# Optimization experiments

Measured on AMD Instinct MI355X. Metric: run time of the kernel, lower is better.

The kernel has to match this reference:

```python
import jax, jax.numpy as jnp
import numpy as np

B, N_NODES, T_IN = 512, 32, 12
HID, HEADS, OUT_CH, DEG = 64, 8, 9, 8


def setup_inputs() -> dict:
    key = jax.random.key(0)
    ks = jax.random.split(key, 26)
    rn = lambda k, s, sc=0.1: (jax.random.normal(k, s, jnp.float32) * sc)
    E = B * N_NODES * DEG
    src = jax.random.randint(ks[0], (E,), 0, N_NODES, jnp.int32)
    dst = jax.random.randint(ks[1], (E,), 0, N_NODES, jnp.int32)
    off = jnp.repeat(jnp.arange(B, dtype=jnp.int32) * N_NODES, N_NODES * DEG)
    edge_index = jnp.stack([src + off, dst + off])  # block-diagonal batched graph
    x = jax.random.normal(ks[2], (B, N_NODES, T_IN), jnp.float32)
    return {
        "x": x,
        "edge_index": edge_index,
        # gat1: in=T_IN -> HEADS*HID, concat
        "W1": rn(ks[3], (T_IN, HEADS * HID)),
        "a_src1": rn(ks[4], (HEADS, HID)),
        "a_dst1": rn(ks[5], (HEADS, HID)),
        "b1": rn(ks[6], (HEADS * HID,), 0.01),
        # gat2: in=HEADS*HID -> HID, heads=1, mean (concat=False)
        "W2": rn(ks[7], (HEADS * HID, HID), 0.05),
        "a_src2": rn(ks[8], (1, HID)),
        "a_dst2": rn(ks[9], (1, HID)),
        "b2": rn(ks[10], (HID,), 0.01),
        "gamma": jnp.ones((HID,), jnp.float32),
        "beta": jnp.zeros((HID,), jnp.float32),
        # gru1: input_size=N_NODES(=32), hidden=HID
        "Wi1": rn(ks[11], (3 * HID, N_NODES)),
        "Wh1": rn(ks[12], (3 * HID, HID)),
        "bi1": rn(ks[13], (3 * HID,), 0.01),
        "bh1": rn(ks[14], (3 * HID,), 0.01),
        # gru2: input_size=HID, hidden=HID
        "Wi2": rn(ks[15], (3 * HID, HID)),
        "Wh2": rn(ks[16], (3 * HID, HID)),
        "bi2": rn(ks[17], (3 * HID,), 0.01),
        "bh2": rn(ks[18], (3 * HID,), 0.01),
        "Wf": rn(ks[19], (OUT_CH, HID)),
        "bf": rn(ks[20], (OUT_CH,), 0.01),
    }


def _gat_layer(x, src, dst, W, a_s, a_d, b, concat):
    # PyG GATConv (eval mode, self-loops already appended by caller)
    Nn = x.shape[0]
    heads, hc = a_s.shape
    h = (x @ W).reshape(Nn, heads, hc)                 # [N, H, C]
    es = jnp.sum(h * a_s, axis=-1)                     # [N, H]
    ed = jnp.sum(h * a_d, axis=-1)
    e = jax.nn.leaky_relu(es[src] + ed[dst], 0.2)      # [E, H]
    m = jax.ops.segment_max(e, dst, num_segments=Nn)
    p = jnp.exp(e - m[dst])
    s = jax.ops.segment_sum(p, dst, num_segments=Nn)
    alpha = p / (s[dst] + 1e-16)                       # per-dst softmax
    out = jax.ops.segment_sum(h[src] * alpha[:, :, None], dst, num_segments=Nn)
    out = out.reshape(Nn, heads * hc) if concat else out.mean(axis=1)
    return out + b


def _gru(x, Wi, Wh, bi, bh):
    # torch.nn.GRU (batch_first) single layer; x: [B, T, F]
    H = Wh.shape[1]
    xi = x @ Wi.T + bi                                 # [B, T, 3H]
    def step(h, xt):
        gh = h @ Wh.T + bh
        r = jax.nn.sigmoid(xt[:, :H] + gh[:, :H])
        z = jax.nn.sigmoid(xt[:, H:2 * H] + gh[:, H:2 * H])
        n = jnp.tanh(xt[:, 2 * H:] + r * gh[:, 2 * H:])
        hn = (1.0 - z) * n + z * h
        return hn, hn
    h0 = jnp.zeros((x.shape[0], H), x.dtype)
    _, ys = jax.lax.scan(step, h0, jnp.swapaxes(xi, 0, 1))
    return jnp.swapaxes(ys, 0, 1)


def reference(x, edge_index, W1, a_src1, a_dst1, b1, W2, a_src2, a_dst2, b2,
              gamma, beta, Wi1, Wh1, bi1, bh1, Wi2, Wh2, bi2, bh2, Wf, bf):
    Bsz, Nn_, T = x.shape
    Nn = Bsz * Nn_
    xf = x.reshape(Nn, T)                              # dropout is identity in eval
    sl = jnp.arange(Nn, dtype=edge_index.dtype)        # PyG add_self_loops=True
    src = jnp.concatenate([edge_index[0], sl])
    dst = jnp.concatenate([edge_index[1], sl])
    h = jax.nn.elu(_gat_layer(xf, src, dst, W1, a_src1, a_dst1, b1, True))
    h = jax.nn.elu(_gat_layer(h, src, dst, W2, a_src2, a_dst2, b2, False))
    mu = h.mean(-1, keepdims=True)
    var = ((h - mu) ** 2).mean(-1, keepdims=True)
    h = (h - mu) / jnp.sqrt(var + 1e-5) * gamma + beta
    seq = h.reshape(Bsz, Nn_, -1).transpose(0, 2, 1)   # [B, HID(seq), N_NODES(feat)]
    g = _gru(seq, Wi1, Wh1, bi1, bh1)
    g = _gru(g, Wi2, Wh2, bi2, bh2)
    return g[:, -1, :] @ Wf.T + bf                     # [B, OUT_CH]
```

## Files before the change

### kernel.cpp

```cpp
#include <hip/hip_runtime.h>
#include <hip/hip_bf16.h>
#include <stdint.h>

#define BATCH 512
#define NN 32
#define T_IN 12
#define HID 64
#define HEADS 8
#define OUT_CH 9
#define EPB (NN*8)
#define ETOT (EPB+NN)
#define F1 (HEADS*HID)

using u16 = unsigned short;
using u32 = unsigned int;
typedef _Float16 f16;
typedef _Float16 f16x2 __attribute__((ext_vector_type(2)));
typedef u32 v4u __attribute__((ext_vector_type(4)));
typedef float v4f __attribute__((ext_vector_type(4)));

__device__ __forceinline__ float bf2f(u16 u){ return __uint_as_float(((u32)u)<<16); }
__device__ __forceinline__ u16 f2bf(float f){
    u32 x = __float_as_uint(f);
    u32 r = (x + 0x7FFFu + ((x>>16)&1u))>>16;
    return (u16)r;
}
__device__ __forceinline__ u32 packf16(float a, float b){
    f16x2 p; p.x=(f16)a; p.y=(f16)b; return __builtin_bit_cast(u32,p);
}
__device__ __forceinline__ u16 f2h16(float a){ f16 h=(f16)a; return __builtin_bit_cast(u16,h); }
__device__ __forceinline__ float h16f(u16 v){ f16 h=__builtin_bit_cast(f16,v); return (float)h; }
__device__ __forceinline__ float lof(u32 w){ return (float)__builtin_bit_cast(f16x2,w).x; }
__device__ __forceinline__ float hif(u32 w){ return (float)__builtin_bit_cast(f16x2,w).y; }
__device__ __forceinline__ float dot2(u32 a, u32 b, float c){
#if __has_builtin(__builtin_amdgcn_fdot2)
    return __builtin_amdgcn_fdot2(__builtin_bit_cast(f16x2,a), __builtin_bit_cast(f16x2,b), c, false);
#else
    return fmaf(lof(a),lof(b), fmaf(hif(a),hif(b), c));
#endif
}
__device__ __forceinline__ float elu1(float x){ return x > 0.f ? x : (__expf(x)-1.f); }
__device__ __forceinline__ float sigm(float x){ return 1.f/(1.f+__expf(-x)); }
__device__ __forceinline__ float tanh_(float x){ return 1.f - 2.f/(__expf(2.f*x)+1.f); }
__device__ __forceinline__ u32 fenc(float v){
    u32 b=__float_as_uint(v);
    return (b&0x80000000u) ? ~b : (b|0x80000000u);
}
__device__ __forceinline__ float fdec(u32 k){
    return __uint_as_float((k&0x80000000u) ? (k&0x7FFFFFFFu) : ~k);
}

#define DOT4(acc,A,W) do{ acc=dot2(A.x,W.x,acc); acc=dot2(A.y,W.y,acc); \
                          acc=dot2(A.z,W.z,acc); acc=dot2(A.w,W.w,acc); }while(0)

struct CvtDesc {
    const void* src[16];
    void*       dst[16];
    int         n[16];
};

__global__ __launch_bounds__(256) void k_setup(
    const u32* __restrict__ xw, CvtDesc d,
    const void* __restrict__ W2src, u16* __restrict__ W2i,
    const void* __restrict__ Wi1, const void* __restrict__ Wh1,
    const void* __restrict__ Wi2, const void* __restrict__ Wh2,
    u32* __restrict__ wpk, int* __restrict__ flag)
{
    __shared__ int cnt;
    if(threadIdx.x==0) cnt=0;
    __syncthreads();
    int c=0;
    for(int i=threadIdx.x;i<4096;i+=256){
        u32 w=xw[i];
        if(w & 0x7FFFFFFFu){
            u32 el=(w>>7)&0xFFu;
            if(el>=0x90u) c++;
        }
    }
    atomicAdd(&cnt,c);
    __syncthreads();
    const int f = (cnt>256) ? 1 : 0;
    if(blockIdx.x==0 && threadIdx.x==0) *flag=f;

    const int bk=blockIdx.x;
    if(bk<128){
        int seg=bk>>3, sub=bk&7;
        const void* s=d.src[seg];
        float* o=(float*)d.dst[seg];
        int n=d.n[seg];
        for(int i=sub*256+threadIdx.x;i<n;i+=2048)
            o[i] = f ? ((const float*)s)[i] : bf2f(((const u16*)s)[i]);
    } else if(bk<256){
        int i=(bk-128)*256+threadIdx.x;
        int k=i>>6, j=i&63;
        float v = f? ((const float*)W2src)[i] : bf2f(((const u16*)W2src)[i]);
        W2i[ (((size_t)(k>>3)*64 + j)<<3) + (k&7) ] = f2h16(v);
    } else {
        int w=(bk-256)*256+threadIdx.x;
        int m=w/6144;
        int rem=w-m*6144;
        int row=rem>>5, kw=rem&31;
        const void* s=(m==0)?Wi1:(m==1)?Wh1:(m==2)?Wi2:Wh2;
        int K=(m==0)?32:64;
        int k0=2*kw, k1=k0+1;
        float v0=0.f, v1=0.f;
        if(k0<K) v0 = f? ((const float*)s)[row*K+k0] : bf2f(((const u16*)s)[row*K+k0]);
        if(k1<K) v1 = f? ((const float*)s)[row*K+k1] : bf2f(((const u16*)s)[row*K+k1]);
        wpk[w]=packf16(v0,v1);
    }
}

__global__ __launch_bounds__(256,2) void k_gat1(
    const float* __restrict__ x, const int* __restrict__ ei,
    const float* __restrict__ W1, const float* __restrict__ a_s, const float* __restrict__ a_d,
    const float* __restrict__ b1, u32* __restrict__ h1g)
{
    const int b = blockIdx.x, t = threadIdx.x;
    __shared__ __align__(16) float s_x[NN][12];
    __shared__ float s_W1[T_IN*F1];
    __shared__ __align__(16) u16 s_h[NN][520];
    __shared__ __align__(16) u32 s_aspk[HEADS*32], s_adpk[HEADS*32];
    __shared__ float s_es[NN][HEADS], s_ed[NN][HEADS];
    __shared__ unsigned char s_src[ETOT], s_dst[ETOT];
    __shared__ float s_al[HEADS][ETOT];
    __shared__ u32 s_mx[NN*HEADS];
    __shared__ float s_sm[NN*HEADS], s_inv[NN*HEADS];
    __shared__ int s_cnt[NN], s_off[NN], s_fil[NN];
    __shared__ short s_lst[ETOT];

    for(int i=t;i<NN*T_IN;i+=256) s_x[i/12][i%12] = x[b*NN*T_IN + i];
    for(int i=t;i<T_IN*F1;i+=256) s_W1[i]=W1[i];
    s_aspk[t]=packf16(a_s[2*t],a_s[2*t+1]);
    s_adpk[t]=packf16(a_d[2*t],a_d[2*t+1]);
    s_mx[t]=0u; s_sm[t]=0.f;
    if(t<EPB){
        s_src[t] = (unsigned char)(ei[b*EPB+t] - b*NN);
        s_dst[t] = (unsigned char)(ei[(size_t)BATCH*EPB + b*EPB+t] - b*NN);
    }
    if(t<NN){ s_src[EPB+t]=s_dst[EPB+t]=(unsigned char)t; s_cnt[t]=0; s_fil[t]=0; }
    __syncthreads();

    {
        v4f Wa0,Wa1,Wa2,Wb0,Wb1,Wb2;
        Wa0.x=s_W1[0*F1+t]; Wa0.y=s_W1[1*F1+t]; Wa0.z=s_W1[2*F1+t]; Wa0.w=s_W1[3*F1+t];
        Wa1.x=s_W1[4*F1+t]; Wa1.y=s_W1[5*F1+t]; Wa1.z=s_W1[6*F1+t]; Wa1.w=s_W1[7*F1+t];
        Wa2.x=s_W1[8*F1+t]; Wa2.y=s_W1[9*F1+t]; Wa2.z=s_W1[10*F1+t]; Wa2.w=s_W1[11*F1+t];
        Wb0.x=s_W1[0*F1+t+256]; Wb0.y=s_W1[1*F1+t+256]; Wb0.z=s_W1[2*F1+t+256]; Wb0.w=s_W1[3*F1+t+256];
        Wb1.x=s_W1[4*F1+t+256]; Wb1.y=s_W1[5*F1+t+256]; Wb1.z=s_W1[6*F1+t+256]; Wb1.w=s_W1[7*F1+t+256];
        Wb2.x=s_W1[8*F1+t+256]; Wb2.y=s_W1[9*F1+t+256]; Wb2.z=s_W1[10*F1+t+256]; Wb2.w=s_W1[11*F1+t+256];
        for(int n=0;n<NN;n++){
            const float4* xp=(const float4*)s_x[n];
            float4 xa=xp[0], xb=xp[1], xc=xp[2];
            float A=0.f,B=0.f;
            A=fmaf(xa.x,Wa0.x,A); A=fmaf(xa.y,Wa0.y,A); A=fmaf(xa.z,Wa0.z,A); A=fmaf(xa.w,Wa0.w,A);
            A=fmaf(xb.x,Wa1.x,A); A=fmaf(xb.y,Wa1.y,A); A=fmaf(xb.z,Wa1.z,A); A=fmaf(xb.w,Wa1.w,A);
            A=fmaf(xc.x,Wa2.x,A); A=fmaf(xc.y,Wa2.y,A); A=fmaf(xc.z,Wa2.z,A); A=fmaf(xc.w,Wa2.w,A);
            B=fmaf(xa.x,Wb0.x,B); B=fmaf(xa.y,Wb0.y,B); B=fmaf(xa.z,Wb0.z,B); B=fmaf(xa.w,Wb0.w,B);
            B=fmaf(xb.x,Wb1.x,B); B=fmaf(xb.y,Wb1.y,B); B=fmaf(xb.z,Wb1.z,B); B=fmaf(xb.w,Wb1.w,B);
            B=fmaf(xc.x,Wb2.x,B); B=fmaf(xc.y,Wb2.y,B); B=fmaf(xc.z,Wb2.z,B); B=fmaf(xc.w,Wb2.w,B);
            s_h[n][t]=f2h16(A); s_h[n][t+256]=f2h16(B);
        }
    }
    for(int e=t;e<ETOT;e+=256) atomicAdd(&s_cnt[s_dst[e]],1);
    __syncthreads();

    {
        int n=t&31, hd=t>>5;
        const v4u* hp=(const v4u*)((const u16*)s_h[n] + hd*64);
        v4u h0=hp[0],h1=hp[1],h2=hp[2],h3=hp[3],h4=hp[4],h5=hp[5],h6=hp[6],h7=hp[7];
        const v4u* ap=(const v4u*)&s_aspk[hd*32];
        const v4u* dp=(const v4u*)&s_adpk[hd*32];
        float e1=0.f,e2=0.f;
        { v4u w=ap[0]; DOT4(e1,h0,w); w=ap[1]; DOT4(e1,h1,w); w=ap[2]; DOT4(e1,h2,w); w=ap[3]; DOT4(e1,h3,w);
          w=ap[4]; DOT4(e1,h4,w); w=ap[5]; DOT4(e1,h5,w); w=ap[6]; DOT4(e1,h6,w); w=ap[7]; DOT4(e1,h7,w); }
        { v4u w=dp[0]; DOT4(e2,h0,w); w=dp[1]; DOT4(e2,h1,w); w=dp[2]; DOT4(e2,h2,w); w=dp[3]; DOT4(e2,h3,w);
          w=dp[4]; DOT4(e2,h4,w); w=dp[5]; DOT4(e2,h5,w); w=dp[6]; DOT4(e2,h6,w); w=dp[7]; DOT4(e2,h7,w); }
        s_es[n][hd]=e1; s_ed[n][hd]=e2;
    }
    if(t==0){ int o=0; for(int i=0;i<NN;i++){ s_off[i]=o; o+=s_cnt[i]; } }
    __syncthreads();

    for(int e=t;e<ETOT;e+=256){
        int d=s_dst[e]; int p=atomicAdd(&s_fil[d],1); s_lst[s_off[d]+p]=(short)e;
    }
    for(int i=t;i<ETOT*HEADS;i+=256){
        int hd=i/ETOT, e=i-hd*ETOT;
        int sr=s_src[e], d=s_dst[e];
        float v = s_es[sr][hd]+s_ed[d][hd];
        v = v>0.f? v : 0.2f*v;
        s_al[hd][e]=v;
        atomicMax(&s_mx[d*8+hd], fenc(v));
    }
    __syncthreads();

    for(int i=t;i<ETOT*HEADS;i+=256){
        int hd=i/ETOT, e=i-hd*ETOT;
        int d=s_dst[e];
        float p=__expf(s_al[hd][e]-fdec(s_mx[d*8+hd]));
        s_al[hd][e]=p;
        atomicAdd(&s_sm[d*8+hd], p);
    }
    __syncthreads();
    s_inv[t]=1.f/(s_sm[t]+1e-16f);
    __syncthreads();

    {
        int d=t&31, hd=t>>5;
        int o=s_off[d], cnt=s_cnt[d];
        float inv=s_inv[d*8+hd];
        size_t obase = ((size_t)(b*NN+d))*256 + hd*32;
        #pragma unroll
        for(int ch=0;ch<2;ch++){
            v4f a0=0,a1=0,a2=0,a3=0,a4=0,a5=0,a6=0,a7=0;
            for(int i=0;i<cnt;i++){
                int e=s_lst[o+i]; float av=s_al[hd][e]; int sr=s_src[e];
                const v4u* hp=(const v4u*)((const u16*)s_h[sr] + hd*64 + ch*32);
                v4u p0=hp[0],p1=hp[1],p2=hp[2],p3=hp[3];
                a0.x=fmaf(av,lof(p0.x),a0.x); a0.y=fmaf(av,hif(p0.x),a0.y);
                a0.z=fmaf(av,lof(p0.y),a0.z); a0.w=fmaf(av,hif(p0.y),a0.w);
                a1.x=fmaf(av,lof(p0.z),a1.x); a1.y=fmaf(av,hif(p0.z),a1.y);
                a1.z=fmaf(av,lof(p0.w),a1.z); a1.w=fmaf(av,hif(p0.w),a1.w);
                a2.x=fmaf(av,lof(p1.x),a2.x); a2.y=fmaf(av,hif(p1.x),a2.y);
                a2.z=fmaf(av,lof(p1.y),a2.z); a2.w=fmaf(av,hif(p1.y),a2.w);
                a3.x=fmaf(av,lof(p1.z),a3.x); a3.y=fmaf(av,hif(p1.z),a3.y);
                a3.z=fmaf(av,lof(p1.w),a3.z); a3.w=fmaf(av,hif(p1.w),a3.w);
                a4.x=fmaf(av,lof(p2.x),a4.x); a4.y=fmaf(av,hif(p2.x),a4.y);
                a4.z=fmaf(av,lof(p2.y),a4.z); a4.w=fmaf(av,hif(p2.y),a4.w);
                a5.x=fmaf(av,lof(p2.z),a5.x); a5.y=fmaf(av,hif(p2.z),a5.y);
                a5.z=fmaf(av,lof(p2.w),a5.z); a5.w=fmaf(av,hif(p2.w),a5.w);
                a6.x=fmaf(av,lof(p3.x),a6.x); a6.y=fmaf(av,hif(p3.x),a6.y);
                a6.z=fmaf(av,lof(p3.y),a6.z); a6.w=fmaf(av,hif(p3.y),a6.w);
                a7.x=fmaf(av,lof(p3.z),a7.x); a7.y=fmaf(av,hif(p3.z),a7.y);
                a7.z=fmaf(av,lof(p3.w),a7.z); a7.w=fmaf(av,hif(p3.w),a7.w);
            }
            const float* bp = b1 + hd*64 + ch*32;
            u32* op = h1g + obase + ch*16;
            op[0] = packf16(elu1(a0.x*inv+bp[0]),  elu1(a0.y*inv+bp[1]));
            op[1] = packf16(elu1(a0.z*inv+bp[2]),  elu1(a0.w*inv+bp[3]));
            op[2] = packf16(elu1(a1.x*inv+bp[4]),  elu1(a1.y*inv+bp[5]));
            op[3] = packf16(elu1(a1.z*inv+bp[6]),  elu1(a1.w*inv+bp[7]));
            op[4] = packf16(elu1(a2.x*inv+bp[8]),  elu1(a2.y*inv+bp[9]));
            op[5] = packf16(elu1(a2.z*inv+bp[10]), elu1(a2.w*inv+bp[11]));
            op[6] = packf16(elu1(a3.x*inv+bp[12]), elu1(a3.y*inv+bp[13]));
            op[7] = packf16(elu1(a3.z*inv+bp[14]), elu1(a3.w*inv+bp[15]));
            op[8] = packf16(elu1(a4.x*inv+bp[16]), elu1(a4.y*inv+bp[17]));
            op[9] = packf16(elu1(a4.z*inv+bp[18]), elu1(a4.w*inv+bp[19]));
            op[10]= packf16(elu1(a5.x*inv+bp[20]), elu1(a5.y*inv+bp[21]));
            op[11]= packf16(elu1(a5.z*inv+bp[22]), elu1(a5.w*inv+bp[23]));
            op[12]= packf16(elu1(a6.x*inv+bp[24]), elu1(a6.y*inv+bp[25]));
            op[13]= packf16(elu1(a6.z*inv+bp[26]), elu1(a6.w*inv+bp[27]));
            op[14]= packf16(elu1(a7.x*inv+bp[28]), elu1(a7.y*inv+bp[29]));
            op[15]= packf16(elu1(a7.z*inv+bp[30]), elu1(a7.w*inv+bp[31]));
        }
    }
}

__global__ __launch_bounds__(256,2) void k_gat2ln(
    const u32* __restrict__ h1g, const int* __restrict__ ei,
    const uint4* __restrict__ W2i, const float* __restrict__ a_s2, const float* __restrict__ a_d2,
    const float* __restrict__ b2, const float* __restrict__ gam, const float* __restrict__ bet,
    float* __restrict__ hlng)
{
    const int b=blockIdx.x, t=threadIdx.x;
    __shared__ __align__(16) u32 s_h1[NN*260];
    __shared__ float s_h2[NN][HID];
    __shared__ float s_es[NN], s_ed[NN];
    __shared__ unsigned char s_src[ETOT], s_dst[ETOT];
    __shared__ float s_al[ETOT];
    __shared__ u32 s_mx[NN];
    __shared__ float s_sm[NN], s_inv[NN];
    __shared__ int s_cnt[NN], s_off[NN], s_fil[NN];
    __shared__ short s_lst[ETOT];

    { const u32* g = h1g + (size_t)b*8192;
      for(int w=t; w<8192; w+=256){ int n=w>>8, c=w&255; s_h1[n*260+c]=g[w]; } }
    if(t<EPB){
        s_src[t]=(unsigned char)(ei[b*EPB+t]-b*NN);
        s_dst[t]=(unsigned char)(ei[(size_t)BATCH*EPB+b*EPB+t]-b*NN);
    }
    if(t<NN){ s_src[EPB+t]=s_dst[EPB+t]=(unsigned char)t;
              s_cnt[t]=0; s_fil[t]=0; s_mx[t]=0u; s_sm[t]=0.f; }
    __syncthreads();

    for(int e=t;e<ETOT;e+=256) atomicAdd(&s_cnt[s_dst[e]],1);
    {
        int n0=(t>>5)<<2, j0=(t&31)<<1;
        const u32* r0=&s_h1[(n0+0)*260];
        const u32* r1=&s_h1[(n0+1)*260];
        const u32* r2=&s_h1[(n0+2)*260];
        const u32* r3=&s_h1[(n0+3)*260];
        float a00=0,a01=0,a10=0,a11=0,a20=0,a21=0,a30=0,a31=0;
        for(int kb=0;kb<64;kb++){
            uint4 A0=*(const uint4*)&r0[kb*4];
            uint4 A1=*(const uint4*)&r1[kb*4];
            uint4 A2=*(const uint4*)&r2[kb*4];
            uint4 A3=*(const uint4*)&r3[kb*4];
            const uint4* wp=&W2i[kb*64+j0];
            uint4 w0=wp[0], w1=wp[1];
            a00=dot2(A0.x,w0.x,a00); a00=dot2(A0.y,w0.y,a00); a00=dot2(A0.z,w0.z,a00); a00=dot2(A0.w,w0.w,a00);
            a01=dot2(A0.x,w1.x,a01); a01=dot2(A0.y,w1.y,a01); a01=dot2(A0.z,w1.z,a01); a01=dot2(A0.w,w1.w,a01);
            a10=dot2(A1.x,w0.x,a10); a10=dot2(A1.y,w0.y,a10); a10=dot2(A1.z,w0.z,a10); a10=dot2(A1.w,w0.w,a10);
            a11=dot2(A1.x,w1.x,a11); a11=dot2(A1.y,w1.y,a11); a11=dot2(A1.z,w1.z,a11); a11=dot2(A1.w,w1.w,a11);
            a20=dot2(A2.x,w0.x,a20); a20=dot2(A2.y,w0.y,a20); a20=dot2(A2.z,w0.z,a20); a20=dot2(A2.w,w0.w,a20);
            a21=dot2(A2.x,w1.x,a21); a21=dot2(A2.y,w1.y,a21); a21=dot2(A2.z,w1.z,a21); a21=dot2(A2.w,w1.w,a21);
            a30=dot2(A3.x,w0.x,a30); a30=dot2(A3.y,w0.y,a30); a30=dot2(A3.z,w0.z,a30); a30=dot2(A3.w,w0.w,a30);
            a31=dot2(A3.x,w1.x,a31); a31=dot2(A3.y,w1.y,a31); a31=dot2(A3.z,w1.z,a31); a31=dot2(A3.w,w1.w,a31);
        }
        s_h2[n0+0][j0]=a00; s_h2[n0+0][j0+1]=a01;
        s_h2[n0+1][j0]=a10; s_h2[n0+1][j0+1]=a11;
        s_h2[n0+2][j0]=a20; s_h2[n0+2][j0+1]=a21;
        s_h2[n0+3][j0]=a30; s_h2[n0+3][j0+1]=a31;
    }
    __syncthreads();

    {
        int n=t>>3, g=t&7;
        float e1=0,e2=0;
        #pragma unroll
        for(int cc=0; cc<8; cc++){
            float hv = s_h2[n][g*8+cc];
            e1 += hv*a_s2[g*8+cc];
            e2 += hv*a_d2[g*8+cc];
        }
        #pragma unroll
        for(int m=1;m<8;m<<=1){ e1 += __shfl_xor(e1,m,64); e2 += __shfl_xor(e2,m,64); }
        if(g==0){ s_es[n]=e1; s_ed[n]=e2; }
    }
    if(t==0){ int o=0; for(int i=0;i<NN;i++){ s_off[i]=o; o+=s_cnt[i]; } }
    __syncthreads();

    for(int e=t;e<ETOT;e+=256){
        int d=s_dst[e]; int p=atomicAdd(&s_fil[d],1); s_lst[s_off[d]+p]=(short)e;
    }
    for(int e=t;e<ETOT;e+=256){
        int d=s_dst[e];
        float v = s_es[s_src[e]] + s_ed[d];
        v = v>0.f? v:0.2f*v;
        s_al[e]=v;
        atomicMax(&s_mx[d], fenc(v));
    }
    __syncthreads();

    for(int e=t;e<ETOT;e+=256){
        int d=s_dst[e];
        float p=__expf(s_al[e]-fdec(s_mx[d]));
        s_al[e]=p;
        atomicAdd(&s_sm[d], p);
    }
    __syncthreads();
    if(t<NN) s_inv[t]=1.f/(s_sm[t]+1e-16f);
    __syncthreads();

    {
        int n=t>>3, g=t&7;
        v4f a0=0, a1=0;
        int o=s_off[n], cnt=s_cnt[n];
        float inv=s_inv[n];
        for(int i=0;i<cnt;i++){
            int e=s_lst[o+i]; float a=s_al[e]; int sr=s_src[e];
            const float4* hp=(const float4*)&s_h2[sr][g*8];
            float4 v0=hp[0], v1=hp[1];
            a0.x=fmaf(a,v0.x,a0.x); a0.y=fmaf(a,v0.y,a0.y); a0.z=fmaf(a,v0.z,a0.z); a0.w=fmaf(a,v0.w,a0.w);
            a1.x=fmaf(a,v1.x,a1.x); a1.y=fmaf(a,v1.y,a1.y); a1.z=fmaf(a,v1.z,a1.z); a1.w=fmaf(a,v1.w,a1.w);
        }
        const float* bp=b2+g*8;
        float v0=elu1(a0.x*inv+bp[0]), v1=elu1(a0.y*inv+bp[1]);
        float v2=elu1(a0.z*inv+bp[2]), v3=elu1(a0.w*inv+bp[3]);
        float v4=elu1(a1.x*inv+bp[4]), v5=elu1(a1.y*inv+bp[5]);
        float v6=elu1(a1.z*inv+bp[6]), v7=elu1(a1.w*inv+bp[7]);
        float sum=v0+v1+v2+v3+v4+v5+v6+v7;
        float sq=v0*v0+v1*v1+v2*v2+v3*v3+v4*v4+v5*v5+v6*v6+v7*v7;
        #pragma unroll
        for(int m=1;m<8;m<<=1){ sum+=__shfl_xor(sum,m,64); sq+=__shfl_xor(sq,m,64); }
        float mu = sum*(1.f/64.f);
        float var = sq*(1.f/64.f) - mu*mu;
        float rs = rsqrtf(var + 1e-5f);
        float* outp = hlng + (size_t)b*HID*NN;
        int c=g*8;
        outp[(c+0)*NN+n]=(v0-mu)*rs*gam[c+0]+bet[c+0];
        outp[(c+1)*NN+n]=(v1-mu)*rs*gam[c+1]+bet[c+1];
        outp[(c+2)*NN+n]=(v2-mu)*rs*gam[c+2]+bet[c+2];
        outp[(c+3)*NN+n]=(v3-mu)*rs*gam[c+3]+bet[c+3];
        outp[(c+4)*NN+n]=(v4-mu)*rs*gam[c+4]+bet[c+4];
        outp[(c+5)*NN+n]=(v5-mu)*rs*gam[c+5]+bet[c+5];
        outp[(c+6)*NN+n]=(v6-mu)*rs*gam[c+6]+bet[c+6];
        outp[(c+7)*NN+n]=(v7-mu)*rs*gam[c+7]+bet[c+7];
    }
}

__global__ __launch_bounds__(256,2) void k_gruf(
    const float* __restrict__ hlng, const u32* __restrict__ wpk,
    const float* __restrict__ bi1, const float* __restrict__ bh1,
    const float* __restrict__ bi2, const float* __restrict__ bh2,
    const float* __restrict__ Wf, const float* __restrict__ bfv,
    void* __restrict__ outp, const int* __restrict__ flag)
{
    const int b=blockIdx.x, t=threadIdx.x;
    const int wave=t>>6, lane=t&63;
    const int layer=wave>>1;
    const int ublk=wave&1;
    const int uu=lane&31, s=lane>>5;
    const int u=ublk*32+uu;

    __shared__ __align__(16) u32 s_x1[64*16];
    __shared__ __align__(16) u32 s_h1[2][32];
    __shared__ __align__(16) u32 s_h2[2][32];
    __shared__ float s_h2f[64];

    { const float2* g=(const float2*)(hlng + (size_t)b*2048);
      for(int w=t;w<1024;w+=256){ float2 v=g[w]; s_x1[w]=packf16(v.x,v.y); } }
    if(t<32){ s_h1[0][t]=0u; s_h1[1][t]=0u; s_h2[0][t]=0u; s_h2[1][t]=0u; }

    u32 wiR[16],wiZ[16],wiN[16],whR[16],whZ[16],whN[16];
    const u32* wiu = wpk + (size_t)(layer*2+0)*6144;
    const u32* whu = wpk + (size_t)(layer*2+1)*6144;
    if(layer==0){
        #pragma unroll
        for(int k=0;k<8;k++){
            wiR[k]=wiu[u*32+s*8+k];
            wiZ[k]=wiu[(64+u)*32+s*8+k];
            wiN[k]=wiu[(128+u)*32+s*8+k];
        }
        #pragma unroll
        for(int k=0;k<16;k++){
            whR[k]=whu[u*32+s*16+k];
            whZ[k]=whu[(64+u)*32+s*16+k];
            whN[k]=whu[(128+u)*32+s*16+k];
        }
    } else {
        #pragma unroll
        for(int k=0;k<16;k++){
            wiR[k]=wiu[u*32+s*16+k];
            wiZ[k]=wiu[(64+u)*32+s*16+k];
            wiN[k]=wiu[(128+u)*32+s*16+k];
            whR[k]=whu[u*32+s*16+k];
            whZ[k]=whu[(64+u)*32+s*16+k];
            whN[k]=whu[(128+u)*32+s*16+k];
        }
    }
    const float* bi = layer? bi2:bi1;
    const float* bh = layer? bh2:bh1;
    float br=bi[u]+bh[u], bz=bi[64+u]+bh[64+u], bxn=bi[128+u], bhn=bh[128+u];
    float h=0.f;
    __syncthreads();

    for(int it=0; it<=64; ++it){
        const int pb=(it-1)&1, cb=it&1;
        bool act;
        float pr=0.f,pz=0.f,pxn=0.f,phn=0.f;
        if(layer==0){
            act=(it<64);
            if(act){
                const u32* xp=&s_x1[it*16+s*8];
                const u32* hp=&s_h1[pb][s*16];
                #pragma unroll
                for(int k=0;k<8;k++){ u32 xv=xp[k]; pr=dot2(xv,wiR[k],pr); pz=dot2(xv,wiZ[k],pz); pxn=dot2(xv,wiN[k],pxn); }
                #pragma unroll
                for(int k=0;k<16;k++){ u32 hv=hp[k]; pr=dot2(hv,whR[k],pr); pz=dot2(hv,whZ[k],pz); phn=dot2(hv,whN[k],phn); }
            }
        } else {
            act=(it>=1);
            if(act){
                const u32* xp=&s_h1[pb][s*16];
                const u32* hp=&s_h2[pb][s*16];
                #pragma unroll
                for(int k=0;k<16;k++){
                    u32 xv=xp[k], hv=hp[k];
                    pr=dot2(xv,wiR[k],pr); pz=dot2(xv,wiZ[k],pz); pxn=dot2(xv,wiN[k],pxn);
                    pr=dot2(hv,whR[k],pr); pz=dot2(hv,whZ[k],pz); phn=dot2(hv,whN[k],phn);
                }
            }
        }
        if(act){
            pr  += __shfl_xor(pr ,32,64);
            pz  += __shfl_xor(pz ,32,64);
            pxn += __shfl_xor(pxn,32,64);
            phn += __shfl_xor(phn,32,64);
            float r=sigm(pr+br), z=sigm(pz+bz);
            float n=tanh_(pxn+bxn + r*(phn+bhn));
            h=(1.f-z)*n + z*h;
            if(s==0){
                u16 hv=f2h16(h);
                if(layer==0) ((u16*)s_h1[cb])[u]=hv;
                else { ((u16*)s_h2[cb])[u]=hv; if(it==64) s_h2f[u]=h; }
            }
        }
        __syncthreads();
    }

    if(t<OUT_CH){
        float acc=bfv[t];
        const float4* wp=(const float4*)(Wf + t*64);
        const float4* hp=(const float4*)s_h2f;
        #pragma unroll
        for(int k=0;k<16;k++){
            float4 w=wp[k], v=hp[k];
            acc += w.x*v.x + w.y*v.y + w.z*v.z + w.w*v.w;
        }
        if(*flag) ((float*)outp)[b*OUT_CH+t]=acc;
        else      ((u16*)outp)[b*OUT_CH+t]=f2bf(acc);
    }
}

extern "C" void kernel_launch(void* const* d_in, const int* in_sizes, int n_in,
                              void* d_out, int out_size, void* d_ws, size_t ws_size,
                              hipStream_t stream)
{
    char* ws=(char*)d_ws;
    int* flag = (int*)ws;
    float* cf = (float*)(ws + 256);
    float* c_x   = cf; cf+=196608;
    float* c_W1  = cf; cf+=6144;
    float* c_as1 = cf; cf+=512;
    float* c_ad1 = cf; cf+=512;
    float* c_b1  = cf; cf+=512;
    float* c_as2 = cf; cf+=64;
    float* c_ad2 = cf; cf+=64;
    float* c_b2  = cf; cf+=64;
    float* c_gam = cf; cf+=64;
    float* c_bet = cf; cf+=64;
    float* c_bi1 = cf; cf+=192;
    float* c_bh1 = cf; cf+=192;
    float* c_bi2 = cf; cf+=192;
    float* c_bh2 = cf; cf+=192;
    float* c_Wf  = cf; cf+=576;
    float* c_bf  = cf; cf+=9;
    uintptr_t p = ((uintptr_t)cf + 255) & ~(uintptr_t)255;
    u16* c_W2i = (u16*)p;
    p = (p + 32768*2 + 255) & ~(uintptr_t)255;
    u32* wpk = (u32*)p;
    p = (p + 24576*4 + 255) & ~(uintptr_t)255;
    u32* h1g = (u32*)p;
    p = (p + (size_t)BATCH*NN*256*4 + 255) & ~(uintptr_t)255;
    float* hlng = (float*)p;

    const int* ei = (const int*)d_in[1];

    CvtDesc d;
    const int srcIdx[16] = {0,2,3,4,5,7,8,9,10,11,14,15,18,19,20,21};
    void* dsts[16] = {c_x,c_W1,c_as1,c_ad1,c_b1,c_as2,c_ad2,c_b2,c_gam,c_bet,
                      c_bi1,c_bh1,c_bi2,c_bh2,c_Wf,c_bf};
    const int ns[16] = {196608,6144,512,512,512,64,64,64,64,64,
                        192,192,192,192,576,9};
    for(int i=0;i<16;i++){ d.src[i]=d_in[srcIdx[i]]; d.dst[i]=dsts[i]; d.n[i]=ns[i]; }

    k_setup  <<<dim3(352),dim3(256),0,stream>>>((const u32*)d_in[0], d,
                                                d_in[6], c_W2i,
                                                d_in[12], d_in[13], d_in[16], d_in[17],
                                                wpk, flag);
    k_gat1   <<<dim3(BATCH),dim3(256),0,stream>>>(c_x,ei,c_W1,c_as1,c_ad1,c_b1,h1g);
    k_gat2ln <<<dim3(BATCH),dim3(256),0,stream>>>(h1g,ei,(const uint4*)c_W2i,c_as2,c_ad2,c_b2,c_gam,c_bet,hlng);
    k_gruf   <<<dim3(BATCH),dim3(256),0,stream>>>(hlng, wpk, c_bi1,c_bh1,c_bi2,c_bh2,
                                                  c_Wf, c_bf, d_out, flag);
}
```

Before: 238.8 us.

## Fuse GAT1, GAT2+LayerNorm and GRU kernels into one per-graph kernel

Merges the three per-batch kernels into a single kernel that keeps intermediates (GAT1 output, normalized GAT2 output) in shared memory instead of round-tripping through global workspace. It reuses the edge CSR lists built for layer 1 in layer 2 and loads W1 straight from global into registers rather than staging it in shared memory. This removes two kernel launches and roughly the global write/read of the intermediate activations. The cost is a longer, heavier kernel with more register pressure (32-word result array) and more shared memory, which could lower occupancy.

```diff
diff --git a/kernel.cpp b/kernel.cpp
--- a/kernel.cpp
+++ b/kernel.cpp
@@ -29,7 +29,6 @@
     f16x2 p; p.x=(f16)a; p.y=(f16)b; return __builtin_bit_cast(u32,p);
 }
 __device__ __forceinline__ u16 f2h16(float a){ f16 h=(f16)a; return __builtin_bit_cast(u16,h); }
-__device__ __forceinline__ float h16f(u16 v){ f16 h=__builtin_bit_cast(f16,v); return (float)h; }
 __device__ __forceinline__ float lof(u32 w){ return (float)__builtin_bit_cast(f16x2,w).x; }
 __device__ __forceinline__ float hif(u32 w){ return (float)__builtin_bit_cast(f16x2,w).y; }
 __device__ __forceinline__ float dot2(u32 a, u32 b, float c){
@@ -110,14 +109,21 @@
     }
 }
 
-__global__ __launch_bounds__(256,2) void k_gat1(
+__global__ __launch_bounds__(256,2) void k_fused(
     const float* __restrict__ x, const int* __restrict__ ei,
     const float* __restrict__ W1, const float* __restrict__ a_s, const float* __restrict__ a_d,
-    const float* __restrict__ b1, u32* __restrict__ h1g)
+    const float* __restrict__ b1,
+    const uint4* __restrict__ W2i, const float* __restrict__ a_s2, const float* __restrict__ a_d2,
+    const float* __restrict__ b2, const float* __restrict__ gam, const float* __restrict__ bet,
+    const u32* __restrict__ wpk,
+    const float* __restrict__ bi1, const float* __restrict__ bh1,
+    const float* __restrict__ bi2, const float* __restrict__ bh2,
+    const float* __restrict__ Wf, const float* __restrict__ bfv,
+    void* __restrict__ outp, const int* __restrict__ flag)
 {
     const int b = blockIdx.x, t = threadIdx.x;
+
     __shared__ __align__(16) float s_x[NN][12];
-    __shared__ float s_W1[T_IN*F1];
     __shared__ __align__(16) u16 s_h[NN][520];
     __shared__ __align__(16) u32 s_aspk[HEADS*32], s_adpk[HEADS*32];
     __shared__ float s_es[NN][HEADS], s_ed[NN][HEADS];
@@ -127,9 +133,13 @@
     __shared__ float s_sm[NN*HEADS], s_inv[NN*HEADS];
     __shared__ int s_cnt[NN], s_off[NN], s_fil[NN];
     __shared__ short s_lst[ETOT];
+    __shared__ float s_h2[NN][HID];
+    __shared__ __align__(16) u32 s_x1[64*16];
+    __shared__ __align__(16) u32 s_g1[2][32];
+    __shared__ __align__(16) u32 s_g2[2][32];
+    __shared__ float s_h2f[64];
 
     for(int i=t;i<NN*T_IN;i+=256) s_x[i/12][i%12] = x[b*NN*T_IN + i];
-    for(int i=t;i<T_IN*F1;i+=256) s_W1[i]=W1[i];
     s_aspk[t]=packf16(a_s[2*t],a_s[2*t+1]);
     s_adpk[t]=packf16(a_d[2*t],a_d[2*t+1]);
     s_mx[t]=0u; s_sm[t]=0.f;
@@ -138,28 +148,26 @@
         s_dst[t] = (unsigned char)(ei[(size_t)BATCH*EPB + b*EPB+t] - b*NN);
     }
     if(t<NN){ s_src[EPB+t]=s_dst[EPB+t]=(unsigned char)t; s_cnt[t]=0; s_fil[t]=0; }
-    __syncthreads();
-
-    {
-        v4f Wa0,Wa1,Wa2,Wb0,Wb1,Wb2;
-        Wa0.x=s_W1[0*F1+t]; Wa0.y=s_W1[1*F1+t]; Wa0.z=s_W1[2*F1+t]; Wa0.w=s_W1[3*F1+t];
-        Wa1.x=s_W1[4*F1+t]; Wa1.y=s_W1[5*F1+t]; Wa1.z=s_W1[6*F1+t]; Wa1.w=s_W1[7*F1+t];
-        Wa2.x=s_W1[8*F1+t]; Wa2.y=s_W1[9*F1+t]; Wa2.z=s_W1[10*F1+t]; Wa2.w=s_W1[11*F1+t];
-        Wb0.x=s_W1[0*F1+t+256]; Wb0.y=s_W1[1*F1+t+256]; Wb0.z=s_W1[2*F1+t+256]; Wb0.w=s_W1[3*F1+t+256];
-        Wb1.x=s_W1[4*F1+t+256]; Wb1.y=s_W1[5*F1+t+256]; Wb1.z=s_W1[6*F1+t+256]; Wb1.w=s_W1[7*F1+t+256];
-        Wb2.x=s_W1[8*F1+t+256]; Wb2.y=s_W1[9*F1+t+256]; Wb2.z=s_W1[10*F1+t+256]; Wb2.w=s_W1[11*F1+t+256];
-        for(int n=0;n<NN;n++){
-            const float4* xp=(const float4*)s_x[n];
-            float4 xa=xp[0], xb=xp[1], xc=xp[2];
-            float A=0.f,B=0.f;
-            A=fmaf(xa.x,Wa0.x,A); A=fmaf(xa.y,Wa0.y,A); A=fmaf(xa.z,Wa0.z,A); A=fmaf(xa.w,Wa0.w,A);
-            A=fmaf(xb.x,Wa1.x,A); A=fmaf(xb.y,Wa1.y,A); A=fmaf(xb.z,Wa1.z,A); A=fmaf(xb.w,Wa1.w,A);
-            A=fmaf(xc.x,Wa2.x,A); A=fmaf(xc.y,Wa2.y,A); A=fmaf(xc.z,Wa2.z,A); A=fmaf(xc.w,Wa2.w,A);
-            B=fmaf(xa.x,Wb0.x,B); B=fmaf(xa.y,Wb0.y,B); B=fmaf(xa.z,Wb0.z,B); B=fmaf(xa.w,Wb0.w,B);
-            B=fmaf(xb.x,Wb1.x,B); B=fmaf(xb.y,Wb1.y,B); B=fmaf(xb.z,Wb1.z,B); B=fmaf(xb.w,Wb1.w,B);
-            B=fmaf(xc.x,Wb2.x,B); B=fmaf(xc.y,Wb2.y,B); B=fmaf(xc.z,Wb2.z,B); B=fmaf(xc.w,Wb2.w,B);
-            s_h[n][t]=f2h16(A); s_h[n][t+256]=f2h16(B);
-        }
+    v4f Wa0,Wa1,Wa2,Wb0,Wb1,Wb2;
+    Wa0.x=W1[0*F1+t]; Wa0.y=W1[1*F1+t]; Wa0.z=W1[2*F1+t]; Wa0.w=W1[3*F1+t];
+    Wa1.x=W1[4*F1+t]; Wa1.y=W1[5*F1+t]; Wa1.z=W1[6*F1+t]; Wa1.w=W1[7*F1+t];
+    Wa2.x=W1[8*F1+t]; Wa2.y=W1[9*F1+t]; Wa2.z=W1[10*F1+t]; Wa2.w=W1[11*F1+t];
+    Wb0.x=W1[0*F1+t+256]; Wb0.y=W1[1*F1+t+256]; Wb0.z=W1[2*F1+t+256]; Wb0.w=W1[3*F1+t+256];
+    Wb1.x=W1[4*F1+t+256]; Wb1.y=W1[5*F1+t+256]; Wb1.z=W1[6*F1+t+256]; Wb1.w=W1[7*F1+t+256];
+    Wb2.x=W1[8*F1+t+256]; Wb2.y=W1[9*F1+t+256]; Wb2.z=W1[10*F1+t+256]; Wb2.w=W1[11*F1+t+256];
+    __syncthreads();
+
+    for(int n=0;n<NN;n++){
+        const float4* xp=(const float4*)s_x[n];
+        float4 xa=xp[0], xb=xp[1], xc=xp[2];
+        float A=0.f,B=0.f;
+        A=fmaf(xa.x,Wa0.x,A); A=fmaf(xa.y,Wa0.y,A); A=fmaf(xa.z,Wa0.z,A); A=fmaf(xa.w,Wa0.w,A);
+        A=fmaf(xb.x,Wa1.x,A); A=fmaf(xb.y,Wa1.y,A); A=fmaf(xb.z,Wa1.z,A); A=fmaf(xb.w,Wa1.w,A);
+        A=fmaf(xc.x,Wa2.x,A); A=fmaf(xc.y,Wa2.y,A); A=fmaf(xc.z,Wa2.z,A); A=fmaf(xc.w,Wa2.w,A);
+        B=fmaf(xa.x,Wb0.x,B); B=fmaf(xa.y,Wb0.y,B); B=fmaf(xa.z,Wb0.z,B); B=fmaf(xa.w,Wb0.w,B);
+        B=fmaf(xb.x,Wb1.x,B); B=fmaf(xb.y,Wb1.y,B); B=fmaf(xb.z,Wb1.z,B); B=fmaf(xb.w,Wb1.w,B);
+        B=fmaf(xc.x,Wb2.x,B); B=fmaf(xc.y,Wb2.y,B); B=fmaf(xc.z,Wb2.z,B); B=fmaf(xc.w,Wb2.w,B);
+        s_h[n][t]=f2h16(A); s_h[n][t+256]=f2h16(B);
     }
     for(int e=t;e<ETOT;e+=256) atomicAdd(&s_cnt[s_dst[e]],1);
     __syncthreads();
@@ -204,17 +212,17 @@
     s_inv[t]=1.f/(s_sm[t]+1e-16f);
     __syncthreads();
 
-    {
-        int d=t&31, hd=t>>5;
-        int o=s_off[d], cnt=s_cnt[d];
-        float inv=s_inv[d*8+hd];
-        size_t obase = ((size_t)(b*NN+d))*256 + hd*32;
+    u32 res[32];
+    const int dA=t&31, hdA=t>>5;
+    {
+        int o=s_off[dA], cnt=s_cnt[dA];
+        float inv=s_inv[dA*8+hdA];
         #pragma unroll
         for(int ch=0;ch<2;ch++){
             v4f a0=0,a1=0,a2=0,a3=0,a4=0,a5=0,a6=0,a7=0;
             for(int i=0;i<cnt;i++){
-                int e=s_lst[o+i]; float av=s_al[hd][e]; int sr=s_src[e];
-                const v4u* hp=(const v4u*)((const u16*)s_h[sr] + hd*64 + ch*32);
+                int e=s_lst[o+i]; float av=s_al[hdA][e]; int sr=s_src[e];
+                const v4u* hp=(const v4u*)((const u16*)s_h[sr] + hdA*64 + ch*32);
                 v4u p0=hp[0],p1=hp[1],p2=hp[2],p3=hp[3];
                 a0.x=fmaf(av,lof(p0.x),a0.x); a0.y=fmaf(av,hif(p0.x),a0.y);
                 a0.z=fmaf(av,lof(p0.y),a0.z); a0.w=fmaf(av,hif(p0.y),a0.w);
@@ -233,62 +241,41 @@
                 a7.x=fmaf(av,lof(p3.z),a7.x); a7.y=fmaf(av,hif(p3.z),a7.y);
                 a7.z=fmaf(av,lof(p3.w),a7.z); a7.w=fmaf(av,hif(p3.w),a7.w);
             }
-            const float* bp = b1 + hd*64 + ch*32;
-            u32* op = h1g + obase + ch*16;
-            op[0] = packf16(elu1(a0.x*inv+bp[0]),  elu1(a0.y*inv+bp[1]));
-            op[1] = packf16(elu1(a0.z*inv+bp[2]),  elu1(a0.w*inv+bp[3]));
-            op[2] = packf16(elu1(a1.x*inv+bp[4]),  elu1(a1.y*inv+bp[5]));
-            op[3] = packf16(elu1(a1.z*inv+bp[6]),  elu1(a1.w*inv+bp[7]));
-            op[4] = packf16(elu1(a2.x*inv+bp[8]),  elu1(a2.y*inv+bp[9]));
-            op[5] = packf16(elu1(a2.z*inv+bp[10]), elu1(a2.w*inv+bp[11]));
-            op[6] = packf16(elu1(a3.x*inv+bp[12]), elu1(a3.y*inv+bp[13]));
-            op[7] = packf16(elu1(a3.z*inv+bp[14]), elu1(a3.w*inv+bp[15]));
-            op[8] = packf16(elu1(a4.x*inv+bp[16]), elu1(a4.y*inv+bp[17]));
-            op[9] = packf16(elu1(a4.z*inv+bp[18]), elu1(a4.w*inv+bp[19]));
-            op[10]= packf16(elu1(a5.x*inv+bp[20]), elu1(a5.y*inv+bp[21]));
-            op[11]= packf16(elu1(a5.z*inv+bp[22]), elu1(a5.w*inv+bp[23]));
-            op[12]= packf16(elu1(a6.x*inv+bp[24]), elu1(a6.y*inv+bp[25]));
-            op[13]= packf16(elu1(a6.z*inv+bp[26]), elu1(a6.w*inv+bp[27]));
-            op[14]= packf16(elu1(a7.x*inv+bp[28]), elu1(a7.y*inv+bp[29]));
-            op[15]= packf16(elu1(a7.z*inv+bp[30]), elu1(a7.w*inv+bp[31]));
-        }
-    }
-}
-
-__global__ __launch_bounds__(256,2) void k_gat2ln(
-    const u32* __restrict__ h1g, const int* __restrict__ ei,
-    const uint4* __restrict__ W2i, const float* __restrict__ a_s2, const float* __restrict__ a_d2,
-    const float* __restrict__ b2, const float* __restrict__ gam, const float* __restrict__ bet,
-    float* __restrict__ hlng)
-{
-    const int b=blockIdx.x, t=threadIdx.x;
-    __shared__ __align__(16) u32 s_h1[NN*260];
-    __shared__ float s_h2[NN][HID];
-    __shared__ float s_es[NN], s_ed[NN];
-    __shared__ unsigned char s_src[ETOT], s_dst[ETOT];
-    __shared__ float s_al[ETOT];
-    __shared__ u32 s_mx[NN];
-    __shared__ float s_sm[NN], s_inv[NN];
-    __shared__ int s_cnt[NN], s_off[NN], s_fil[NN];
-    __shared__ short s_lst[ETOT];
-
-    { const u32* g = h1g + (size_t)b*8192;
-      for(int w=t; w<8192; w+=256){ int n=w>>8, c=w&255; s_h1[n*260+c]=g[w]; } }
-    if(t<EPB){
-        s_src[t]=(unsigned char)(ei[b*EPB+t]-b*NN);
-        s_dst[t]=(unsigned char)(ei[(size_t)BATCH*EPB+b*EPB+t]-b*NN);
-    }
-    if(t<NN){ s_src[EPB+t]=s_dst[EPB+t]=(unsigned char)t;
-              s_cnt[t]=0; s_fil[t]=0; s_mx[t]=0u; s_sm[t]=0.f; }
-    __syncthreads();
-
-    for(int e=t;e<ETOT;e+=256) atomicAdd(&s_cnt[s_dst[e]],1);
+            const float* bp = b1 + hdA*64 + ch*32;
+            u32* rp = res + ch*16;
+            rp[0] = packf16(elu1(a0.x*inv+bp[0]),  elu1(a0.y*inv+bp[1]));
+            rp[1] = packf16(elu1(a0.z*inv+bp[2]),  elu1(a0.w*inv+bp[3]));
+            rp[2] = packf16(elu1(a1.x*inv+bp[4]),  elu1(a1.y*inv+bp[5]));
+            rp[3] = packf16(elu1(a1.z*inv+bp[6]),  elu1(a1.w*inv+bp[7]));
+            rp[4] = packf16(elu1(a2.x*inv+bp[8]),  elu1(a2.y*inv+bp[9]));
+            rp[5] = packf16(elu1(a2.z*inv+bp[10]), elu1(a2.w*inv+bp[11]));
+            rp[6] = packf16(elu1(a3.x*inv+bp[12]), elu1(a3.y*inv+bp[13]));
+            rp[7] = packf16(elu1(a3.z*inv+bp[14]), elu1(a3.w*inv+bp[15]));
+            rp[8] = packf16(elu1(a4.x*inv+bp[16]), elu1(a4.y*inv+bp[17]));
+            rp[9] = packf16(elu1(a4.z*inv+bp[18]), elu1(a4.w*inv+bp[19]));
+            rp[10]= packf16(elu1(a5.x*inv+bp[20]), elu1(a5.y*inv+bp[21]));
+            rp[11]= packf16(elu1(a5.z*inv+bp[22]), elu1(a5.w*inv+bp[23]));
+            rp[12]= packf16(elu1(a6.x*inv+bp[24]), elu1(a6.y*inv+bp[25]));
+            rp[13]= packf16(elu1(a6.z*inv+bp[26]), elu1(a6.w*inv+bp[27]));
+            rp[14]= packf16(elu1(a7.x*inv+bp[28]), elu1(a7.y*inv+bp[29]));
+            rp[15]= packf16(elu1(a7.z*inv+bp[30]), elu1(a7.w*inv+bp[31]));
+        }
+    }
+    __syncthreads();
+    {
+        u32* rw = ((u32*)s_h) + dA*260 + hdA*32;
+        #pragma unroll
+        for(int i=0;i<32;i++) rw[i]=res[i];
+    }
+    if(t<NN){ s_fil[t]=0; s_mx[t]=0u; s_sm[t]=0.f; }
+    __syncthreads();
+
     {
         int n0=(t>>5)<<2, j0=(t&31)<<1;
-        const u32* r0=&s_h1[(n0+0)*260];
-        const u32* r1=&s_h1[(n0+1)*260];
-        const u32* r2=&s_h1[(n0+2)*260];
-        const u32* r3=&s_h1[(n0+3)*260];
+        const u32* r0=((const u32*)s_h)+(n0+0)*260;
+        const u32* r1=((const u32*)s_h)+(n0+1)*260;
+        const u32* r2=((const u32*)s_h)+(n0+2)*260;
+        const u32* r3=((const u32*)s_h)+(n0+3)*260;
         float a00=0,a01=0,a10=0,a11=0,a20=0,a21=0,a30=0,a31=0;
         for(int kb=0;kb<64;kb++){
             uint4 A0=*(const uint4*)&r0[kb*4];
@@ -324,27 +311,23 @@
         }
         #pragma unroll
         for(int m=1;m<8;m<<=1){ e1 += __shfl_xor(e1,m,64); e2 += __shfl_xor(e2,m,64); }
-        if(g==0){ s_es[n]=e1; s_ed[n]=e2; }
-    }
-    if(t==0){ int o=0; for(int i=0;i<NN;i++){ s_off[i]=o; o+=s_cnt[i]; } }
-    __syncthreads();
-
-    for(int e=t;e<ETOT;e+=256){
-        int d=s_dst[e]; int p=atomicAdd(&s_fil[d],1); s_lst[s_off[d]+p]=(short)e;
-    }
+        if(g==0){ s_es[n][0]=e1; s_ed[n][0]=e2; }
+    }
+    __syncthreads();
+
     for(int e=t;e<ETOT;e+=256){
         int d=s_dst[e];
-        float v = s_es[s_src[e]] + s_ed[d];
+        float v = s_es[s_src[e]][0] + s_ed[d][0];
         v = v>0.f? v:0.2f*v;
-        s_al[e]=v;
+        s_al[0][e]=v;
         atomicMax(&s_mx[d], fenc(v));
     }
     __syncthreads();
 
     for(int e=t;e<ETOT;e+=256){
         int d=s_dst[e];
-        float p=__expf(s_al[e]-fdec(s_mx[d]));
-        s_al[e]=p;
+        float p=__expf(s_al[0][e]-fdec(s_mx[d]));
+        s_al[0][e]=p;
         atomicAdd(&s_sm[d], p);
     }
     __syncthreads();
@@ -357,7 +340,7 @@
         int o=s_off[n], cnt=s_cnt[n];
         float inv=s_inv[n];
         for(int i=0;i<cnt;i++){
-            int e=s_lst[o+i]; float a=s_al[e]; int sr=s_src[e];
+            int e=s_lst[o+i]; float a=s_al[0][e]; int sr=s_src[e];
             const float4* hp=(const float4*)&s_h2[sr][g*8];
             float4 v0=hp[0], v1=hp[1];
             a0.x=fmaf(a,v0.x,a0.x); a0.y=fmaf(a,v0.y,a0.y); a0.z=fmaf(a,v0.z,a0.z); a0.w=fmaf(a,v0.w,a0.w);
@@ -375,117 +358,102 @@
         float mu = sum*(1.f/64.f);
         float var = sq*(1.f/64.f) - mu*mu;
         float rs = rsqrtf(var + 1e-5f);
-        float* outp = hlng + (size_t)b*HID*NN;
+        u16* xw=(u16*)s_x1;
         int c=g*8;
-        outp[(c+0)*NN+n]=(v0-mu)*rs*gam[c+0]+bet[c+0];
-        outp[(c+1)*NN+n]=(v1-mu)*rs*gam[c+1]+bet[c+1];
-        outp[(c+2)*NN+n]=(v2-mu)*rs*gam[c+2]+bet[c+2];
-        outp[(c+3)*NN+n]=(v3-mu)*rs*gam[c+3]+bet[c+3];
-        outp[(c+4)*NN+n]=(v4-mu)*rs*gam[c+4]+bet[c+4];
-        outp[(c+5)*NN+n]=(v5-mu)*rs*gam[c+5]+bet[c+5];
-        outp[(c+6)*NN+n]=(v6-mu)*rs*gam[c+6]+bet[c+6];
-        outp[(c+7)*NN+n]=(v7-mu)*rs*gam[c+7]+bet[c+7];
-    }
-}
-
-__global__ __launch_bounds__(256,2) void k_gruf(
-    const float* __restrict__ hlng, const u32* __restrict__ wpk,
-    const float* __restrict__ bi1, const float* __restrict__ bh1,
-    const float* __restrict__ bi2, const float* __restrict__ bh2,
-    const float* __restrict__ Wf, const float* __restrict__ bfv,
-    void* __restrict__ outp, const int* __restrict__ flag)
-{
-    const int b=blockIdx.x, t=threadIdx.x;
-    const int wave=t>>6, lane=t&63;
-    const int layer=wave>>1;
-    const int ublk=wave&1;
-    const int uu=lane&31, s=lane>>5;
-    const int u=ublk*32+uu;
-
-    __shared__ __align__(16) u32 s_x1[64*16];
-    __shared__ __align__(16) u32 s_h1[2][32];
-    __shared__ __align__(16) u32 s_h2[2][32];
-    __shared__ float s_h2f[64];
-
-    { const float2* g=(const float2*)(hlng + (size_t)b*2048);
-      for(int w=t;w<1024;w+=256){ float2 v=g[w]; s_x1[w]=packf16(v.x,v.y); } }
-    if(t<32){ s_h1[0][t]=0u; s_h1[1][t]=0u; s_h2[0][t]=0u; s_h2[1][t]=0u; }
-
-    u32 wiR[16],wiZ[16],wiN[16],whR[16],whZ[16],whN[16];
-    const u32* wiu = wpk + (size_t)(layer*2+0)*6144;
-    const u32* whu = wpk + (size_t)(layer*2+1)*6144;
-    if(layer==0){
-        #pragma unroll
-        for(int k=0;k<8;k++){
-            wiR[k]=wiu[u*32+s*8+k];
-            wiZ[k]=wiu[(64+u)*32+s*8+k];
-            wiN[k]=wiu[(128+u)*32+s*8+k];
-        }
-        #pragma unroll
-        for(int k=0;k<16;k++){
-            whR[k]=whu[u*32+s*16+k];
-            whZ[k]=whu[(64+u)*32+s*16+k];
-            whN[k]=whu[(128+u)*32+s*16+k];
-        }
-    } else {
-        #pragma unroll
-        for(int k=0;k<16;k++){
-            wiR[k]=wiu[u*32+s*16+k];
-            wiZ[k]=wiu[(64+u)*32+s*16+k];
-            wiN[k]=wiu[(128+u)*32+s*16+k];
-            whR[k]=whu[u*32+s*16+k];
-            whZ[k]=whu[(64+u)*32+s*16+k];
-            whN[k]=whu[(128+u)*32+s*16+k];
-        }
-    }
-    const float* bi = layer? bi2:bi1;
-    const float* bh = layer? bh2:bh1;
-    float br=bi[u]+bh[u], bz=bi[64+u]+bh[64+u], bxn=bi[128+u], bhn=bh[128+u];
-    float h=0.f;
-    __syncthreads();
-
-    for(int it=0; it<=64; ++it){
-        const int pb=(it-1)&1, cb=it&1;
-        bool act;
-        float pr=0.f,pz=0.f,pxn=0.f,phn=0.f;
+        xw[(c+0)*NN+n]=f2h16((v0-mu)*rs*gam[c+0]+bet[c+0]);
+        xw[(c+1)*NN+n]=f2h16((v1-mu)*rs*gam[c+1]+bet[c+1]);
+        xw[(c+2)*NN+n]=f2h16((v2-mu)*rs*gam[c+2]+bet[c+2]);
+        xw[(c+3)*NN+n]=f2h16((v3-mu)*rs*gam[c+3]+bet[c+3]);
+        xw[(c+4)*NN+n]=f2h16((v4-mu)*rs*gam[c+4]+bet[c+4]);
+        xw[(c+5)*NN+n]=f2h16((v5-mu)*rs*gam[c+5]+bet[c+5]);
+        xw[(c+6)*NN+n]=f2h16((v6-mu)*rs*gam[c+6]+bet[c+6]);
+        xw[(c+7)*NN+n]=f2h16((v7-mu)*rs*gam[c+7]+bet[c+7]);
+    }
+    if(t<32){ s_g1[0][t]=0u; s_g1[1][t]=0u; s_g2[0][t]=0u; s_g2[1][t]=0u; }
+    __syncthreads();
+
+    {
+        const int wave=t>>6, lane=t&63;
+        const int layer=wave>>1;
+        const int ublk=wave&1;
+        const int uu=lane&31, s=lane>>5;
+        const int u=ublk*32+uu;
+
+        u32 wiR[16],wiZ[16],wiN[16],whR[16],whZ[16],whN[16];
+        const u32* wiu = wpk + (size_t)(layer*2+0)*6144;
+        const u32* whu = wpk + (size_t)(layer*2+1)*6144;
         if(layer==0){
-            act=(it<64);
-            if(act){
-                const u32* xp=&s_x1[it*16+s*8];
-                const u32* hp=&s_h1[pb][s*16];
-                #pragma unroll
-                for(int k=0;k<8;k++){ u32 xv=xp[k]; pr=dot2(xv,wiR[k],pr); pz=dot2(xv,wiZ[k],pz); pxn=dot2(xv,wiN[k],pxn); }
-                #pragma unroll
-                for(int k=0;k<16;k++){ u32 hv=hp[k]; pr=dot2(hv,whR[k],pr); pz=dot2(hv,whZ[k],pz); phn=dot2(hv,whN[k],phn); }
+            #pragma unroll
+            for(int k=0;k<8;k++){
+                wiR[k]=wiu[u*32+s*8+k];
+                wiZ[k]=wiu[(64+u)*32+s*8+k];
+                wiN[k]=wiu[(128+u)*32+s*8+k];
+            }
+            #pragma unroll
+            for(int k=0;k<16;k++){
+                whR[k]=whu[u*32+s*16+k];
+                whZ[k]=whu[(64+u)*32+s*16+k];
+                whN[k]=whu[(128+u)*32+s*16+k];
             }
         } else {
-            act=(it>=1);
-            if(act){
-                const u32* xp=&s_h1[pb][s*16];
-                const u32* hp=&s_h2[pb][s*16];
-                #pragma unroll
-                for(int k=0;k<16;k++){
-                    u32 xv=xp[k], hv=hp[k];
-                    pr=dot2(xv,wiR[k],pr); pz=dot2(xv,wiZ[k],pz); pxn=dot2(xv,wiN[k],pxn);
-                    pr=dot2(hv,whR[k],pr); pz=dot2(hv,whZ[k],pz); phn=dot2(hv,whN[k],phn);
+            #pragma unroll
+            for(int k=0;k<16;k++){
+                wiR[k]=wiu[u*32+s*16+k];
+                wiZ[k]=wiu[(64+u)*32+s*16+k];
+                wiN[k]=wiu[(128+u)*32+s*16+k];
+                whR[k]=whu[u*32+s*16+k];
+                whZ[k]=whu[(64+u)*32+s*16+k];
+                whN[k]=whu[(128+u)*32+s*16+k];
+            }
+        }
+        const float* bi = layer? bi2:bi1;
+        const float* bh = layer? bh2:bh1;
+        float br=bi[u]+bh[u], bz=bi[64+u]+bh[64+u], bxn=bi[128+u], bhn=bh[128+u];
+        float h=0.f;
+
+        for(int it=0; it<=64; ++it){
+            const int pb=(it-1)&1, cb=it&1;
+            bool act;
+            float pr=0.f,pz=0.f,pxn=0.f,phn=0.f;
+            if(layer==0){
+                act=(it<64);
+                if(act){
+                    const u32* xp=&s_x1[it*16+s*8];
+                    const u32* hp=&s_g1[pb][s*16];
+                    #pragma unroll
+                    for(int k=0;k<8;k++){ u32 xv=xp[k]; pr=dot2(xv,wiR[k],pr); pz=dot2(xv,wiZ[k],pz); pxn=dot2(xv,wiN[k],pxn); }
+                    #pragma unroll
+                    for(int k=0;k<16;k++){ u32 hv=hp[k]; pr=dot2(hv,whR[k],pr); pz=dot2(hv,whZ[k],pz); phn=dot2(hv,whN[k],phn); }
+                }
+            } else {
+                act=(it>=1);
+                if(act){
+                    const u32* xp=&s_g1[pb][s*16];
+                    const u32* hp=&s_g2[pb][s*16];
+                    #pragma unroll
+                    for(int k=0;k<16;k++){
+                        u32 xv=xp[k], hv=hp[k];
+                        pr=dot2(xv,wiR[k],pr); pz=dot2(xv,wiZ[k],pz); pxn=dot2(xv,wiN[k],pxn);
+                        pr=dot2(hv,whR[k],pr); pz=dot2(hv,whZ[k],pz); phn=dot2(hv,whN[k],phn);
+                    }
                 }
             }
-        }
-        if(act){
-            pr  += __shfl_xor(pr ,32,64);
-            pz  += __shfl_xor(pz ,32,64);
-            pxn += __shfl_xor(pxn,32,64);
-            phn += __shfl_xor(phn,32,64);
-            float r=sigm(pr+br), z=sigm(pz+bz);
-            float n=tanh_(pxn+bxn + r*(phn+bhn));
-            h=(1.f-z)*n + z*h;
-            if(s==0){
-                u16 hv=f2h16(h);
-                if(layer==0) ((u16*)s_h1[cb])[u]=hv;
-                else { ((u16*)s_h2[cb])[u]=hv; if(it==64) s_h2f[u]=h; }
+            if(act){
+                pr  += __shfl_xor(pr ,32,64);
+                pz  += __shfl_xor(pz ,32,64);
+                pxn += __shfl_xor(pxn,32,64);
+                phn += __shfl_xor(phn,32,64);
+                float r=sigm(pr+br), z=sigm(pz+bz);
+                float n=tanh_(pxn+bxn + r*(phn+bhn));
+                h=(1.f-z)*n + z*h;
+                if(s==0){
+                    u16 hv=f2h16(h);
+                    if(layer==0) ((u16*)s_g1[cb])[u]=hv;
+                    else { ((u16*)s_g2[cb])[u]=hv; if(it==64) s_h2f[u]=h; }
+                }
             }
-        }
-        __syncthreads();
+            __syncthreads();
+        }
     }
 
     if(t<OUT_CH){
@@ -529,10 +497,6 @@
     u16* c_W2i = (u16*)p;
     p = (p + 32768*2 + 255) & ~(uintptr_t)255;
     u32* wpk = (u32*)p;
-    p = (p + 24576*4 + 255) & ~(uintptr_t)255;
-    u32* h1g = (u32*)p;
-    p = (p + (size_t)BATCH*NN*256*4 + 255) & ~(uintptr_t)255;
-    float* hlng = (float*)p;
 
     const int* ei = (const int*)d_in[1];
 
@@ -544,12 +508,13 @@
                         192,192,192,192,576,9};
     for(int i=0;i<16;i++){ d.src[i]=d_in[srcIdx[i]]; d.dst[i]=dsts[i]; d.n[i]=ns[i]; }
 
-    k_setup  <<<dim3(352),dim3(256),0,stream>>>((const u32*)d_in[0], d,
-                                                d_in[6], c_W2i,
-                                                d_in[12], d_in[13], d_in[16], d_in[17],
-                                                wpk, flag);
-    k_gat1   <<<dim3(BATCH),dim3(256),0,stream>>>(c_x,ei,c_W1,c_as1,c_ad1,c_b1,h1g);
-    k_gat2ln <<<dim3(BATCH),dim3(256),0,stream>>>(h1g,ei,(const uint4*)c_W2i,c_as2,c_ad2,c_b2,c_gam,c_bet,hlng);
-    k_gruf   <<<dim3(BATCH),dim3(256),0,stream>>>(hlng, wpk, c_bi1,c_bh1,c_bi2,c_bh2,
-                                                  c_Wf, c_bf, d_out, flag);
-}
+    k_setup <<<dim3(352),dim3(256),0,stream>>>((const u32*)d_in[0], d,
+                                               d_in[6], c_W2i,
+                                               d_in[12], d_in[13], d_in[16], d_in[17],
+                                               wpk, flag);
+    k_fused <<<dim3(BATCH),dim3(256),0,stream>>>(
+        c_x, ei, c_W1, c_as1, c_ad1, c_b1,
+        (const uint4*)c_W2i, c_as2, c_ad2, c_b2, c_gam, c_bet,
+        wpk, c_bi1, c_bh1, c_bi2, c_bh2,
+        c_Wf, c_bf, d_out, flag);
+}
```

Measured after the change: 219.8 us. 7.9% less time.
